# Kernel tuning notes

Hardware: AMD Instinct MI355X
Metric: run time of the kernel (lower is better)

## Reference

```python
import jax, jax.numpy as jnp
import numpy as np

DIM = 384
H = 64
W = 64
NB = 8
BS = DIM // NB
WF = W // 2 + 1
EPS = 1e-5


def _layernorm(x, g, b):
    mu = jnp.mean(x, axis=-1, keepdims=True)
    var = jnp.mean(jnp.square(x - mu), axis=-1, keepdims=True)
    return (x - mu) * jax.lax.rsqrt(var + EPS) * g + b


def setup_inputs() -> dict:
    key = jax.random.key(0)
    ks = jax.random.split(key, 8)
    scale = 0.02
    x = jax.random.normal(ks[0], (8, H, W, DIM), dtype=jnp.float32)
    # complex params stored as real view (..., 2) like torch.view_as_real
    w1 = scale * jax.random.normal(ks[1], (H, WF, NB, BS, BS, 2), dtype=jnp.float32)
    b1 = scale * jax.random.normal(ks[2], (H, WF, NB, BS, 2), dtype=jnp.float32)
    norm1_w = jnp.ones((DIM,), jnp.float32)
    norm1_b = jnp.zeros((DIM,), jnp.float32)
    norm2_w = jnp.ones((DIM,), jnp.float32)
    norm2_b = jnp.zeros((DIM,), jnp.float32)
    lim1 = 1.0 / np.sqrt(DIM)
    lim2 = 1.0 / np.sqrt(4 * DIM)
    mlp_w1 = jax.random.uniform(ks[3], (DIM, 4 * DIM), jnp.float32, -lim1, lim1)
    mlp_b1 = jax.random.uniform(ks[4], (4 * DIM,), jnp.float32, -lim1, lim1)
    mlp_w2 = jax.random.uniform(ks[5], (4 * DIM, DIM), jnp.float32, -lim2, lim2)
    mlp_b2 = jax.random.uniform(ks[6], (DIM,), jnp.float32, -lim2, lim2)
    return {"x": x, "w1": w1, "b1": b1, "norm1_w": norm1_w, "norm1_b": norm1_b,
            "norm2_w": norm2_w, "norm2_b": norm2_b, "mlp_w1": mlp_w1, "mlp_b1": mlp_b1,
            "mlp_w2": mlp_w2, "mlp_b2": mlp_b2}


def reference(x, w1, b1, norm1_w, norm1_b, norm2_w, norm2_b, mlp_w1, mlp_b1, mlp_w2, mlp_b2):
    B, h, w, C = x.shape
    residual = x
    xn = _layernorm(x, norm1_w, norm1_b)
    # spectral token mixing (fp32, ortho norm)
    xf = jnp.fft.rfft2(xn.astype(jnp.float32), axes=(1, 2), norm="ortho")  # (B,H,WF,C) complex
    xf = xf.reshape(B, h, w // 2 + 1, NB, BS)
    w1c = jax.lax.complex(w1[..., 0], w1[..., 1])  # (H,WF,NB,BS,BS)
    b1c = jax.lax.complex(b1[..., 0], b1[..., 1])  # (H,WF,NB,BS)
    o1 = jnp.einsum("bhwni,hwnio->bhwno", xf, w1c) + b1c
    o1 = jax.lax.complex(jax.nn.relu(o1.real), jax.nn.relu(o1.imag))
    o1 = o1.reshape(B, h, w // 2 + 1, C)
    xs = jnp.fft.irfft2(o1, s=(h, w), axes=(1, 2), norm="ortho")  # (B,H,W,C) real
    # channel MLP (dropout in eval mode = identity), exact GELU as torch default
    xm = _layernorm(xs, norm2_w, norm2_b)
    hdn = jax.nn.gelu(xm @ mlp_w1 + mlp_b1, approximate=False)
    mlp_out = hdn @ mlp_w2 + mlp_b2
    return xs + residual + mlp_out
```

## Files before the change

### kernel.cpp

```cpp
#include <hip/hip_runtime.h>
#include <math.h>


#define BB 8
#define CC 384
#define WF 33
#define NBK 8
#define BSZ 48
#define NTOK 32768
#define TW64 0.09817477042468103f

#define T_AWF 0
#define T_AHF 5120
#define T_AHI 21504
#define T_AWI 37888

typedef __attribute__((ext_vector_type(8))) short bf16x8;
typedef __attribute__((ext_vector_type(4))) float f32x4;

__device__ __forceinline__ unsigned short f2b(float f) {
  union { float f; unsigned u; } x; x.f = f;
  unsigned u = x.u;
  return (unsigned short)((u + 0x7fffu + ((u >> 16) & 1u)) >> 16);
}
__device__ __forceinline__ float b2fl(unsigned short u) {
  return __uint_as_float(((unsigned)u) << 16);
}
__device__ __forceinline__ void gload16(const void* g, void* l) {
  __builtin_amdgcn_global_load_lds(
      (const __attribute__((address_space(1))) void*)g,
      (__attribute__((address_space(3))) void*)l, 16, 0, 0);
}

__global__ __launch_bounds__(256) void prep_kernel(unsigned short* __restrict__ A,
    const float* __restrict__ mw1, unsigned short* __restrict__ w1t,
    const float* __restrict__ mw2, unsigned short* __restrict__ w2t) {
  __shared__ float tile[32][33];
  int bid = blockIdx.x;
  if (bid < 64) {
    int idx0 = bid * 256 + threadIdx.x;
    const float S = 0.125f;
    for (int e = idx0; e < 5120; e += 16384) {
      int m = e >> 6, w = e & 63;
      float val = 0.f;
      if (m < 66) {
        int kwv = m >> 1;
        float th = (float)((kwv * w) & 63) * TW64;
        val = (m & 1) ? (((kwv==0)||(kwv==32)) ? 0.f : -sinf(th)*S) : cosf(th)*S;
      }
      A[T_AWF + e] = f2b(val);
    }
    for (int e = idx0; e < 16384; e += 16384) {
      int comp = e >> 13; int r = e & 8191; int mp = r >> 6, hh = r & 63;
      int cpo = mp >> 6, kh = mp & 63;
      float th = (float)((kh * hh) & 63) * TW64;
      float cv = cosf(th), sv = sinf(th);
      float fv = (cpo == 0) ? (comp == 0 ? cv : sv) : (comp == 0 ? -sv : cv);
      A[T_AHF + e] = f2b(fv * S);
      float iv = (cpo == 0) ? (comp == 0 ? cv : -sv) : (comp == 0 ? sv : cv);
      A[T_AHI + e] = f2b(iv * S);
    }
    for (int e = idx0; e < 4096; e += 16384) {
      int w = e >> 6, kp = e & 63;
      float val;
      if (kp <= 32) {
        float th = (float)((kp * w) & 63) * TW64;
        val = cosf(th) * (((kp==0)||(kp==32)) ? 1.f : 2.f) * S;
      } else {
        int k2 = kp - 32;
        float th = (float)((k2 * w) & 63) * TW64;
        val = -2.f * sinf(th) * S;
      }
      A[T_AWI + e] = f2b(val);
    }
    return;
  }
  const float* in; unsigned short* outb; int R, C, tb;
  if (bid < 640) { in = mw1; outb = w1t; R = 384; C = 1536; tb = bid - 64; }
  else           { in = mw2; outb = w2t; R = 1536; C = 384; tb = bid - 640; }
  int ntc = C >> 5;
  int bx = tb % ntc;
  int by = tb / ntc;
  int tx = threadIdx.x & 31, ty = threadIdx.x >> 5;
  for (int rr2 = ty; rr2 < 32; rr2 += 8)
    tile[rr2][tx] = in[(size_t)(by*32+rr2)*C + bx*32 + tx];
  __syncthreads();
  for (int rr2 = ty; rr2 < 32; rr2 += 8)
    outb[(size_t)(bx*32+rr2)*R + by*32 + tx] = f2b(tile[tx][rr2]);
}

__global__ __launch_bounds__(256) void ln1t_kernel(const float* __restrict__ x,
    const float* __restrict__ g, const float* __restrict__ be,
    unsigned short* __restrict__ xn) {
  int outer = blockIdx.x;
  int tid = threadIdx.x, lane = tid & 63, wg = tid >> 6;
  const float* base = x + (size_t)outer * 64 * 384;
  float s[16], s2[16];
#pragma unroll
  for (int q = 0; q < 16; ++q) { s[q] = 0.f; s2[q] = 0.f; }
  for (int ch = 0; ch < 6; ++ch) {
#pragma unroll
    for (int q = 0; q < 16; ++q) {
      float v = base[(size_t)(wg*16 + q)*384 + ch*64 + lane];
      s[q] += v; s2[q] += v*v;
    }
  }
#pragma unroll
  for (int q = 0; q < 16; ++q) {
#pragma unroll
    for (int off = 32; off >= 1; off >>= 1) {
      s[q] += __shfl_xor(s[q], off);
      s2[q] += __shfl_xor(s2[q], off);
    }
  }
  float mu[16], rs[16];
#pragma unroll
  for (int q = 0; q < 16; ++q) {
    mu[q] = s[q] * (1.f/384.f);
    rs[q] = rsqrtf(s2[q] * (1.f/384.f) - mu[q]*mu[q] + 1e-5f);
  }
  unsigned short* o = xn + (size_t)outer * 384 * 64;
  for (int ch = 0; ch < 6; ++ch) {
    int c = ch*64 + lane;
    float ga = g[c], bb2 = be[c];
#pragma unroll
    for (int qq = 0; qq < 4; ++qq) {
      unsigned short hv[4];
#pragma unroll
      for (int r2 = 0; r2 < 4; ++r2) {
        int q = qq*4 + r2;
        hv[r2] = f2b((base[(size_t)(wg*16+q)*384 + c]-mu[q])*rs[q]*ga + bb2);
      }
      uint2 pw;
      pw.x = hv[0] | ((unsigned)hv[1] << 16);
      pw.y = hv[2] | ((unsigned)hv[3] << 16);
      *(uint2*)(o + (size_t)c*64 + wg*16 + qq*4) = pw;
    }
  }
}

template<int STAGE>
__global__ __launch_bounds__(256) void dft_kernel(
    const unsigned short* __restrict__ A0, const unsigned short* __restrict__ D,
    unsigned short* __restrict__ O) {
  constexpr int M = (STAGE==0) ? 80 : (STAGE==3) ? 64 : 128;
  constexpr int MT = M / 16;
  constexpr int NA = (STAGE==1 || STAGE==2) ? 2 : 1;
  constexpr int ABYTES = NA * M * 128;
  constexpr int STG = ABYTES + 16384;
  constexpr int EPB = 64 * 128 * 4;
  constexpr int SB = (STG > EPB) ? STG : EPB;
  __shared__ __align__(16) char smem[SB];
  char* BPL = smem + ABYTES;

  int bid = blockIdx.x;
  int cc = bid % 3; int outer = bid / 3;
  int c0 = cc * 128;
  int tid = threadIdx.x, lane = tid & 63, wid = tid >> 6;
  int rr = lane & 15, rq = lane >> 4;
  int b, h = 0, kw = 0;
  if (STAGE == 0 || STAGE == 3) { b = outer >> 6; h = outer & 63; }
  else { b = outer / 33; kw = outer % 33; }

  f32x4 acc[MT][2];
#pragma unroll
  for (int mt = 0; mt < MT; ++mt)
#pragma unroll
    for (int nt = 0; nt < 2; ++nt) acc[mt][nt] = (f32x4){0.f,0.f,0.f,0.f};

  const unsigned short* Atab =
    (STAGE==0) ? A0+T_AWF : (STAGE==1) ? A0+T_AHF : (STAGE==2) ? A0+T_AHI : A0+T_AWI;
  constexpr int ACH = NA * M * 8;
#pragma unroll
  for (int i = 0; i < (ACH + 255)/256; ++i) {
    int t2 = tid + i*256;
    if ((ACH % 256 == 0) || (t2 < ACH)) {
      int mm = t2 >> 3, ch = t2 & 7;
      gload16(Atab + mm*64 + ((ch ^ (mm & 7)) << 3), smem + i*4096 + wid*1024);
    }
  }

  int ncomp = (STAGE == 1) ? ((kw == 0 || kw == 32) ? 1 : 2) : NA;

  for (int comp = 0; comp < ncomp; ++comp) {
    if (comp) __syncthreads();
    if (STAGE == 0) {
      const unsigned short* src = D + (((size_t)(b*64 + h))*384 + c0) * 64;
#pragma unroll
      for (int i = 0; i < 4; ++i) {
        int idx = tid + i*256;
        int c = idx >> 3, ch = idx & 7;
        gload16(src + c*64 + ((ch ^ (c & 7)) << 3), BPL + i*4096 + wid*1024);
      }
    } else {
      size_t P; int RS;
      if (STAGE == 1) { P = (size_t)b*(64*66*384) + (size_t)(2*kw + comp)*384 + c0; RS = 66*384; }
      else if (STAGE == 2) { P = ((size_t)((b*2 + comp)*33) + kw)*64*384 + c0; RS = 384; }
      else { P = (size_t)b*(64*64*384) + (size_t)h*384 + c0; RS = 64*384; }
      const unsigned short* p0 = D + P;
#pragma unroll
      for (int i = 0; i < 4; ++i) {
        int kq = (tid >> 6) + i*4;
        int c2 = (tid & 63) * 2;
        const unsigned short* p = p0 + (size_t)(4*kq)*RS + c2;
        unsigned u0 = *(const unsigned*)p;
        unsigned u1 = *(const unsigned*)(p + RS);
        unsigned u2 = *(const unsigned*)(p + 2*(size_t)RS);
        unsigned u3 = *(const unsigned*)(p + 3*(size_t)RS);
        uint2 w0, w1v;
        w0.x = (u0 & 0xffffu) | (u1 << 16);
        w0.y = (u2 & 0xffffu) | (u3 << 16);
        w1v.x = (u0 >> 16) | (u1 & 0xffff0000u);
        w1v.y = (u2 >> 16) | (u3 & 0xffff0000u);
        *(uint2*)(BPL + c2*128 + ((kq*8) ^ ((c2 & 7) << 4))) = w0;
        *(uint2*)(BPL + (c2+1)*128 + ((kq*8) ^ (((c2+1) & 7) << 4))) = w1v;
      }
    }
    __syncthreads();
#pragma unroll
    for (int kh2 = 0; kh2 < 2; ++kh2) {
      int chb = kh2*4 + rq;
      bf16x8 bfr[2];
#pragma unroll
      for (int nt = 0; nt < 2; ++nt) {
        int n = wid*32 + nt*16 + rr;
        bfr[nt] = *(const bf16x8*)(BPL + n*128 + ((chb ^ (n & 7)) << 4));
      }
#pragma unroll
      for (int mt = 0; mt < MT; ++mt) {
        int mr = mt*16 + rr;
        bf16x8 af = *(const bf16x8*)(smem + comp*(M*128) + mr*128 + ((chb ^ (mr & 7)) << 4));
#pragma unroll
        for (int nt = 0; nt < 2; ++nt)
          acc[mt][nt] = __builtin_amdgcn_mfma_f32_16x16x32_bf16(af, bfr[nt], acc[mt][nt], 0, 0, 0);
      }
    }
  }
  __syncthreads();

  float* ep = (float*)smem;
  constexpr int NHM = (M + 63) / 64;
#pragma unroll
  for (int hm = 0; hm < NHM; ++hm) {
    if (hm) __syncthreads();
#pragma unroll
    for (int mo = 0; mo < 4; ++mo) {
      int mt = hm*4 + mo;
      if (mt >= MT) break;
#pragma unroll
      for (int nt = 0; nt < 2; ++nt)
#pragma unroll
        for (int j = 0; j < 4; ++j) {
          int m2 = mo*16 + rq*4 + j;
          int cl = wid*32 + nt*16 + rr;
          ep[m2*128 + (cl ^ ((m2 & 7) << 2))] = acc[mt][nt][j];
        }
    }
    __syncthreads();
    for (int it = tid; it < 64*16; it += 256) {
      int m2 = it >> 4, u8 = it & 15;
      int m = hm*64 + m2;
      if (m >= M) break;
      if (STAGE == 0 && m >= 66) break;
      if (STAGE == 2) { int cp = m >> 6; if (cp && (kw == 0 || kw == 32)) continue; }
      int swz = (m2 & 7) << 2;
      float4 v0 = *(const float4*)(ep + m2*128 + ((u8*8) ^ swz));
      float4 v1 = *(const float4*)(ep + m2*128 + ((u8*8 + 4) ^ swz));
      uint4 pw;
      pw.x = f2b(v0.x) | ((unsigned)f2b(v0.y) << 16);
      pw.y = f2b(v0.z) | ((unsigned)f2b(v0.w) << 16);
      pw.z = f2b(v1.x) | ((unsigned)f2b(v1.y) << 16);
      pw.w = f2b(v1.z) | ((unsigned)f2b(v1.w) << 16);
      size_t rowb;
      if (STAGE == 0) rowb = ((size_t)(b*64 + h)*66 + m)*384 + c0;
      else if (STAGE == 1) { int cp = m >> 6, kh = m & 63;
        rowb = (((size_t)((b*2 + cp)*64 + kh)*33) + kw)*384 + c0; }
      else if (STAGE == 2) { int cp = m >> 6, h2 = m & 63; int kp = cp ? 32 + kw : kw;
        rowb = ((size_t)(b*64 + kp)*64 + h2)*384 + c0; }
      else rowb = ((size_t)(b*64 + h)*64 + m)*384 + c0;
      *(uint4*)(O + rowb + u8*8) = pw;
    }
  }
}

__global__ __launch_bounds__(384) void blockmm2_kernel(
    const unsigned short* __restrict__ S2, const float* __restrict__ w1,
    const float* __restrict__ b1, unsigned short* __restrict__ o1) {
  int bid = blockIdx.x;
  int np = bid % 4;
  int kw = (bid / 4) % WF;
  int h = bid / (4*WF);
  int tid = threadIdx.x;
  __shared__ float4 wl4[2][48*24];
  __shared__ float2 xl[2][BB][48];
  __shared__ float2 bl[2][48];
#pragma unroll
  for (int e = tid; e < 2304; e += 384) {
    int sub = e / 1152, r = e % 1152;
    const float4* wb4 = (const float4*)(w1 + ((size_t)((h*WF + kw)*NBK) + 2*np + sub)*(BSZ*BSZ*2));
    wl4[sub][r] = wb4[r];
  }
  if (tid < 96) {
    int sub = tid / 48, o = tid % 48;
    bl[sub][o] = ((const float2*)b1)[((size_t)((h*WF + kw)*NBK) + 2*np + sub)*BSZ + o];
  }
#pragma unroll
  for (int e = tid; e < 768; e += 384) {
    int sub = e / 384, r = e % 384, bb = r / 48, i = r % 48;
    int n = 2*np + sub;
    size_t ir = (((size_t)((bb*2 + 0)*64 + h)*33) + kw)*384 + n*48 + i;
    size_t ii = (((size_t)((bb*2 + 1)*64 + h)*33) + kw)*384 + n*48 + i;
    xl[sub][bb][i] = make_float2(b2fl(S2[ir]), b2fl(S2[ii]));
  }
  __syncthreads();
  int sub = tid / 192, r = tid % 192, bb = r / 24, o2 = r % 24;
  float4 bv = *(const float4*)(&bl[sub][2*o2]);
  float2 a0 = make_float2(bv.x, bv.y);
  float2 a1 = make_float2(bv.z, bv.w);
#pragma unroll
  for (int i = 0; i < 48; ++i) {
    float2 xv = xl[sub][bb][i];
    float4 wv = wl4[sub][i*24 + o2];
    a0.x += xv.x*wv.x - xv.y*wv.y;
    a0.y += xv.x*wv.y + xv.y*wv.x;
    a1.x += xv.x*wv.z - xv.y*wv.w;
    a1.y += xv.x*wv.w + xv.y*wv.z;
  }
  int n = 2*np + sub;
  size_t idr = (((size_t)((bb*2 + 0)*33) + kw)*64 + h)*384 + n*48 + 2*o2;
  size_t idi = (((size_t)((bb*2 + 1)*33) + kw)*64 + h)*384 + n*48 + 2*o2;
  *(unsigned*)(o1 + idr) = f2b(fmaxf(a0.x, 0.f)) | ((unsigned)f2b(fmaxf(a1.x, 0.f)) << 16);
  *(unsigned*)(o1 + idi) = f2b(fmaxf(a0.y, 0.f)) | ((unsigned)f2b(fmaxf(a1.y, 0.f)) << 16);
}

__global__ __launch_bounds__(256) void ln2_kernel(const unsigned short* __restrict__ in,
    const float* __restrict__ g, const float* __restrict__ bsh,
    unsigned short* __restrict__ outp) {
  int token = blockIdx.x * 4 + (threadIdx.x >> 6);
  int lane = threadIdx.x & 63;
  const unsigned short* row = in + (size_t)token * CC;
  float v[6]; float s = 0.f;
#pragma unroll
  for (int j = 0; j < 6; ++j) { v[j] = b2fl(row[lane + 64*j]); s += v[j]; }
#pragma unroll
  for (int off = 32; off >= 1; off >>= 1) s += __shfl_xor(s, off);
  float mu = s * (1.0f/CC);
  float q = 0.f;
#pragma unroll
  for (int j = 0; j < 6; ++j) { float d = v[j] - mu; q += d*d; }
#pragma unroll
  for (int off = 32; off >= 1; off >>= 1) q += __shfl_xor(q, off);
  float rs = rsqrtf(q * (1.0f/CC) + 1e-5f);
#pragma unroll
  for (int j = 0; j < 6; ++j) {
    int c = lane + 64*j;
    outp[(size_t)token*CC + c] = f2b((v[j]-mu)*rs*g[c] + bsh[c]);
  }
}

template<int MODE>
__global__ __launch_bounds__(256) void mfma_gemm_kernel(
    const unsigned short* __restrict__ A, int lda,
    const unsigned short* __restrict__ BT, int ldbt,
    const float* __restrict__ bias,
    void* __restrict__ Cp, int ldc, int K, int ntn,
    const unsigned short* __restrict__ xsb, const float* __restrict__ xres,
    const float* __restrict__ b2v) {
  __shared__ __align__(16) unsigned short gsm[128*64*2];
  unsigned short* As = gsm;
  unsigned short* Bs = gsm + 128*64;
  int nb = (int)gridDim.x;
  int bidx = (int)blockIdx.x;
  int bswz = (bidx & 7) * (nb >> 3) + (bidx >> 3);
  int bn = bswz % ntn;
  int bm = bswz / ntn;
  int t = threadIdx.x;
  int lane = t & 63;
  int wid = t >> 6;
  int wm = wid >> 1, wn = wid & 1;
  int rr = lane & 15, rq = lane >> 4;

  f32x4 acc[4][4];
#pragma unroll
  for (int m = 0; m < 4; ++m)
#pragma unroll
    for (int n = 0; n < 4; ++n) acc[m][n] = (f32x4){0.f,0.f,0.f,0.f};

  const unsigned short* Abase = A + (size_t)bm*128*lda;
  const unsigned short* Bbase = BT + (size_t)bn*128*ldbt;

  for (int k0 = 0; k0 < K; k0 += 64) {
#pragma unroll
    for (int i = 0; i < 4; ++i) {
      int idx = t + i*256;
      int row = idx >> 3, ch = idx & 7;
      gload16(Abase + (size_t)row*lda + k0 + ((ch ^ (row & 7)) << 3),
              (char*)As + i*4096 + wid*1024);
    }
#pragma unroll
    for (int i = 0; i < 4; ++i) {
      int idx = t + i*256;
      int row = idx >> 3, ch = idx & 7;
      gload16(Bbase + (size_t)row*ldbt + k0 + ((ch ^ (row & 7)) << 3),
              (char*)Bs + i*4096 + wid*1024);
    }
    __syncthreads();
#pragma unroll
    for (int ks = 0; ks < 2; ++ks) {
      int chb = ks*4 + rq;
      bf16x8 af[4], bfr[4];
#pragma unroll
      for (int m = 0; m < 4; ++m) {
        int row = wm*64 + m*16 + rr;
        af[m] = *(const bf16x8*)((const char*)As + row*128 + ((chb ^ (row & 7)) << 4));
      }
#pragma unroll
      for (int n = 0; n < 4; ++n) {
        int row = wn*64 + n*16 + rr;
        bfr[n] = *(const bf16x8*)((const char*)Bs + row*128 + ((chb ^ (row & 7)) << 4));
      }
#pragma unroll
      for (int m = 0; m < 4; ++m)
#pragma unroll
        for (int n = 0; n < 4; ++n)
          acc[m][n] = __builtin_amdgcn_mfma_f32_16x16x32_bf16(af[m], bfr[n], acc[m][n], 0, 0, 0);
    }
    __syncthreads();
  }

  if (MODE == 0) {
    unsigned short* ep = gsm;
#pragma unroll
    for (int m = 0; m < 4; ++m)
#pragma unroll
      for (int n = 0; n < 4; ++n)
#pragma unroll
        for (int j = 0; j < 4; ++j) {
          int row = wm*64 + m*16 + rq*4 + j;
          int col = wn*64 + n*16 + rr;
          float v = acc[m][n][j];
          v += bias[bn*128 + col];
          v = 0.5f*v*(1.f + erff(v*0.70710678118654752f));
          ep[row*128 + (col ^ ((row & 7) << 3))] = f2b(v);
        }
    __syncthreads();
    for (int it = t; it < 128*16; it += 256) {
      int m = it >> 4, u8 = it & 15;
      uint4 pw = *(const uint4*)(ep + m*128 + ((u8*8) ^ ((m & 7) << 3)));
      *(uint4*)((unsigned short*)Cp + (size_t)(bm*128 + m)*ldc + bn*128 + u8*8) = pw;
    }
  } else {
    float* ep = (float*)gsm;
#pragma unroll
    for (int half = 0; half < 2; ++half) {
      __syncthreads();
#pragma unroll
      for (int mo = 0; mo < 2; ++mo) {
        int m = half*2 + mo;
#pragma unroll
        for (int n = 0; n < 4; ++n)
#pragma unroll
          for (int j = 0; j < 4; ++j) {
            int lr = wm*32 + mo*16 + rq*4 + j;
            int col = wn*64 + n*16 + rr;
            ep[lr*128 + (col ^ ((lr & 7) << 2))] = acc[m][n][j];
          }
      }
      __syncthreads();
      for (int it = t; it < 64*32; it += 256) {
        int lr = it >> 5, u = it & 31;
        int swz = (lr & 7) << 2;
        float4 v = *(const float4*)(ep + lr*128 + ((u*4) ^ swz));
        int grow = bm*128 + (lr >> 5)*64 + (half*2 + ((lr >> 4) & 1))*16 + (lr & 15);
        int gcol = bn*128 + u*4;
        size_t idx = (size_t)grow*ldc + gcol;
        float4 xr = *(const float4*)(xres + idx);
        uint2 xsv = *(const uint2*)(xsb + idx);
        float4 bv = *(const float4*)(b2v + gcol);
        float4 ov;
        ov.x = v.x + xr.x + b2fl((unsigned short)(xsv.x & 0xffffu)) + bv.x;
        ov.y = v.y + xr.y + b2fl((unsigned short)(xsv.x >> 16)) + bv.y;
        ov.z = v.z + xr.z + b2fl((unsigned short)(xsv.y & 0xffffu)) + bv.z;
        ov.w = v.w + xr.w + b2fl((unsigned short)(xsv.y >> 16)) + bv.w;
        *(float4*)((float*)Cp + idx) = ov;
      }
    }
  }
}

extern "C" void kernel_launch(void* const* d_in, const int* in_sizes, int n_in,
                              void* d_out, int out_size, void* d_ws, size_t ws_size,
                              hipStream_t stream) {
  const float* x   = (const float*)d_in[0];
  const float* w1  = (const float*)d_in[1];
  const float* b1  = (const float*)d_in[2];
  const float* n1w = (const float*)d_in[3];
  const float* n1b = (const float*)d_in[4];
  const float* n2w = (const float*)d_in[5];
  const float* n2b = (const float*)d_in[6];
  const float* mw1 = (const float*)d_in[7];
  const float* mb1 = (const float*)d_in[8];
  const float* mw2 = (const float*)d_in[9];
  const float* mb2 = (const float*)d_in[10];
  float* out = (float*)d_out;

  char* ws = (char*)d_ws;
  const size_t MB = 1ull << 20;
  unsigned short* xn  = (unsigned short*)(ws + 0*MB);
  unsigned short* S1  = (unsigned short*)(ws + 26*MB);
  unsigned short* S2  = (unsigned short*)(ws + 53*MB);
  unsigned short* o1  = (unsigned short*)(ws + 80*MB);
  unsigned short* S3  = (unsigned short*)(ws + 107*MB);
  unsigned short* xsb = (unsigned short*)(ws + 133*MB);
  unsigned short* xmb = (unsigned short*)(ws + 159*MB);
  unsigned short* hid = (unsigned short*)(ws + 185*MB);
  unsigned short* w1t = (unsigned short*)(ws + 286*MB);
  unsigned short* w2t = (unsigned short*)(ws + 288*MB);
  unsigned short* atab = (unsigned short*)(ws + 290*MB);

  prep_kernel<<<1216, 256, 0, stream>>>(atab, mw1, w1t, mw2, w2t);

  ln1t_kernel<<<512, 256, 0, stream>>>(x, n1w, n1b, xn);
  dft_kernel<0><<<512*3, 256, 0, stream>>>(atab, xn, S1);
  dft_kernel<1><<<264*3, 256, 0, stream>>>(atab, S1, S2);
  blockmm2_kernel<<<64*WF*4, 384, 0, stream>>>(S2, w1, b1, o1);
  dft_kernel<2><<<264*3, 256, 0, stream>>>(atab, o1, S3);
  dft_kernel<3><<<512*3, 256, 0, stream>>>(atab, S3, xsb);
  ln2_kernel<<<NTOK/4, 256, 0, stream>>>(xsb, n2w, n2b, xmb);
  mfma_gemm_kernel<0><<<256*12, 256, 0, stream>>>(xmb, 384, w1t, 384, mb1,
                                                  hid, 1536, 384, 12,
                                                  nullptr, nullptr, nullptr);
  mfma_gemm_kernel<1><<<256*3, 256, 0, stream>>>(hid, 1536, w2t, 1536, nullptr,
                                                 out, 384, 1536, 3,
                                                 xsb, x, mb2);
}
```

Baseline: 386.3 us.

## Fold LayerNorm2 into MLP GEMM epilogue and double-buffer GEMM K loop

Replaces the ln2 kernel, which wrote a normalized bf16 tensor, with a stats-only kernel that stores per-token mean and rstd. The first GEMM now reads the raw xsb directly. The gamma scaling is folded into the transposed W1 weights, and gamma·W1 column sums plus the beta/bias term are precomputed in prep, so normalization is applied algebraically in the GEMM epilogue. The GEMM main loop also changes from single-buffered 64-wide K tiles to double-buffered 32-wide tiles, overlapping loads with MFMA. This removes one full activation write/read pass, at the cost of using E[x²]-μ² for variance and a serial 384-step column-sum loop in prep.

```diff
diff --git a/kernel.cpp b/kernel.cpp
--- a/kernel.cpp
+++ b/kernel.cpp
@@ -34,7 +34,9 @@
 
 __global__ __launch_bounds__(256) void prep_kernel(unsigned short* __restrict__ A,
     const float* __restrict__ mw1, unsigned short* __restrict__ w1t,
-    const float* __restrict__ mw2, unsigned short* __restrict__ w2t) {
+    const float* __restrict__ mw2, unsigned short* __restrict__ w2t,
+    const float* __restrict__ n2w, const float* __restrict__ n2b,
+    const float* __restrict__ mb1, float2* __restrict__ gsbb) {
   __shared__ float tile[32][33];
   int bid = blockIdx.x;
   if (bid < 64) {
@@ -75,9 +77,22 @@
     }
     return;
   }
-  const float* in; unsigned short* outb; int R, C, tb;
-  if (bid < 640) { in = mw1; outb = w1t; R = 384; C = 1536; tb = bid - 64; }
-  else           { in = mw2; outb = w2t; R = 1536; C = 384; tb = bid - 640; }
+  if (bid >= 1216) {
+    int n0 = (bid - 1216) * 256 + threadIdx.x;
+    if (n0 < 1536) {
+      float gsv = 0.f, bbv = 0.f;
+      for (int k = 0; k < 384; ++k) {
+        float a = mw1[(size_t)k*1536 + n0];
+        gsv += n2w[k]*a;
+        bbv += n2b[k]*a;
+      }
+      gsbb[n0] = make_float2(gsv, bbv + mb1[n0]);
+    }
+    return;
+  }
+  const float* in; unsigned short* outb; int R, C, tb; bool fold;
+  if (bid < 640) { in = mw1; outb = w1t; R = 384; C = 1536; tb = bid - 64; fold = true; }
+  else           { in = mw2; outb = w2t; R = 1536; C = 384; tb = bid - 640; fold = false; }
   int ntc = C >> 5;
   int bx = tb % ntc;
   int by = tb / ntc;
@@ -85,8 +100,9 @@
   for (int rr2 = ty; rr2 < 32; rr2 += 8)
     tile[rr2][tx] = in[(size_t)(by*32+rr2)*C + bx*32 + tx];
   __syncthreads();
+  float gv = fold ? n2w[by*32 + tx] : 1.f;
   for (int rr2 = ty; rr2 < 32; rr2 += 8)
-    outb[(size_t)(bx*32+rr2)*R + by*32 + tx] = f2b(tile[tx][rr2]);
+    outb[(size_t)(bx*32+rr2)*R + by*32 + tx] = f2b(tile[tx][rr2] * gv);
 }
 
 __global__ __launch_bounds__(256) void ln1t_kernel(const float* __restrict__ x,
@@ -333,28 +349,26 @@
   *(unsigned*)(o1 + idi) = f2b(fmaxf(a0.y, 0.f)) | ((unsigned)f2b(fmaxf(a1.y, 0.f)) << 16);
 }
 
-__global__ __launch_bounds__(256) void ln2_kernel(const unsigned short* __restrict__ in,
-    const float* __restrict__ g, const float* __restrict__ bsh,
-    unsigned short* __restrict__ outp) {
+__global__ __launch_bounds__(256) void stats_kernel(const unsigned short* __restrict__ in,
+    float2* __restrict__ stats) {
   int token = blockIdx.x * 4 + (threadIdx.x >> 6);
   int lane = threadIdx.x & 63;
   const unsigned short* row = in + (size_t)token * CC;
-  float v[6]; float s = 0.f;
-#pragma unroll
-  for (int j = 0; j < 6; ++j) { v[j] = b2fl(row[lane + 64*j]); s += v[j]; }
-#pragma unroll
-  for (int off = 32; off >= 1; off >>= 1) s += __shfl_xor(s, off);
-  float mu = s * (1.0f/CC);
-  float q = 0.f;
-#pragma unroll
-  for (int j = 0; j < 6; ++j) { float d = v[j] - mu; q += d*d; }
-#pragma unroll
-  for (int off = 32; off >= 1; off >>= 1) q += __shfl_xor(q, off);
-  float rs = rsqrtf(q * (1.0f/CC) + 1e-5f);
+  float s = 0.f, s2 = 0.f;
 #pragma unroll
   for (int j = 0; j < 6; ++j) {
-    int c = lane + 64*j;
-    outp[(size_t)token*CC + c] = f2b((v[j]-mu)*rs*g[c] + bsh[c]);
+    float v = b2fl(row[lane + 64*j]);
+    s += v; s2 += v*v;
+  }
+#pragma unroll
+  for (int off = 32; off >= 1; off >>= 1) {
+    s += __shfl_xor(s, off);
+    s2 += __shfl_xor(s2, off);
+  }
+  if (lane == 0) {
+    float mu = s * (1.0f/CC);
+    float rs = rsqrtf(s2 * (1.0f/CC) - mu*mu + 1e-5f);
+    stats[token] = make_float2(mu, rs);
   }
 }
 
@@ -362,13 +376,11 @@
 __global__ __launch_bounds__(256) void mfma_gemm_kernel(
     const unsigned short* __restrict__ A, int lda,
     const unsigned short* __restrict__ BT, int ldbt,
-    const float* __restrict__ bias,
     void* __restrict__ Cp, int ldc, int K, int ntn,
+    const float2* __restrict__ stats, const float2* __restrict__ gsbb,
     const unsigned short* __restrict__ xsb, const float* __restrict__ xres,
     const float* __restrict__ b2v) {
-  __shared__ __align__(16) unsigned short gsm[128*64*2];
-  unsigned short* As = gsm;
-  unsigned short* Bs = gsm + 128*64;
+  __shared__ __align__(16) char gsm[32768];
   int nb = (int)gridDim.x;
   int bidx = (int)blockIdx.x;
   int bswz = (bidx & 7) * (nb >> 3) + (bidx >> 3);
@@ -388,61 +400,79 @@
 
   const unsigned short* Abase = A + (size_t)bm*128*lda;
   const unsigned short* Bbase = BT + (size_t)bn*128*ldbt;
-
-  for (int k0 = 0; k0 < K; k0 += 64) {
-#pragma unroll
-    for (int i = 0; i < 4; ++i) {
-      int idx = t + i*256;
-      int row = idx >> 3, ch = idx & 7;
-      gload16(Abase + (size_t)row*lda + k0 + ((ch ^ (row & 7)) << 3),
-              (char*)As + i*4096 + wid*1024);
-    }
-#pragma unroll
-    for (int i = 0; i < 4; ++i) {
-      int idx = t + i*256;
-      int row = idx >> 3, ch = idx & 7;
-      gload16(Bbase + (size_t)row*ldbt + k0 + ((ch ^ (row & 7)) << 3),
-              (char*)Bs + i*4096 + wid*1024);
-    }
+  int nt = K >> 5;
+
+#define STG(bsel, t0)                                                        \
+  {                                                                          \
+    _Pragma("unroll")                                                        \
+    for (int i = 0; i < 2; ++i) {                                            \
+      int u = t + i*256;                                                     \
+      int row = u >> 2, ch = u & 3;                                          \
+      gload16(Abase + (size_t)row*lda + (t0)*32 + ((ch ^ (row & 3)) << 3),   \
+              gsm + (bsel)*16384 + i*4096 + wid*1024);                       \
+      gload16(Bbase + (size_t)row*ldbt + (t0)*32 + ((ch ^ (row & 3)) << 3),  \
+              gsm + (bsel)*16384 + 8192 + i*4096 + wid*1024);                \
+    }                                                                        \
+  }
+
+#define CMP(bsel)                                                            \
+  {                                                                          \
+    const char* Ab2 = gsm + (bsel)*16384;                                    \
+    const char* Bb2 = Ab2 + 8192;                                            \
+    bf16x8 af[4], bfv[4];                                                    \
+    _Pragma("unroll")                                                        \
+    for (int m = 0; m < 4; ++m) {                                            \
+      int row = wm*64 + m*16 + rr;                                           \
+      af[m] = *(const bf16x8*)(Ab2 + row*64 + ((rq ^ (row & 3)) << 4));      \
+    }                                                                        \
+    _Pragma("unroll")                                                        \
+    for (int n = 0; n < 4; ++n) {                                            \
+      int row = wn*64 + n*16 + rr;                                           \
+      bfv[n] = *(const bf16x8*)(Bb2 + row*64 + ((rq ^ (row & 3)) << 4));     \
+    }                                                                        \
+    _Pragma("unroll")                                                        \
+    for (int m = 0; m < 4; ++m)                                              \
+      _Pragma("unroll")                                                      \
+      for (int n = 0; n < 4; ++n)                                            \
+        acc[m][n] = __builtin_amdgcn_mfma_f32_16x16x32_bf16(af[m], bfv[n], acc[m][n], 0, 0, 0); \
+  }
+
+  STG(0, 0);
+  __syncthreads();
+  int cur = 0;
+  for (int tt = 0; tt < nt - 1; ++tt) {
+    STG(cur ^ 1, tt + 1);
+    CMP(cur);
     __syncthreads();
-#pragma unroll
-    for (int ks = 0; ks < 2; ++ks) {
-      int chb = ks*4 + rq;
-      bf16x8 af[4], bfr[4];
-#pragma unroll
-      for (int m = 0; m < 4; ++m) {
-        int row = wm*64 + m*16 + rr;
-        af[m] = *(const bf16x8*)((const char*)As + row*128 + ((chb ^ (row & 7)) << 4));
-      }
+    cur ^= 1;
+  }
+  CMP(cur);
+  __syncthreads();
+
+#undef STG
+#undef CMP
+
+  if (MODE == 0) {
+    unsigned short* ep = (unsigned short*)gsm;
+#pragma unroll
+    for (int m = 0; m < 4; ++m) {
+      float2 st[4];
+#pragma unroll
+      for (int j = 0; j < 4; ++j)
+        st[j] = stats[bm*128 + wm*64 + m*16 + rq*4 + j];
 #pragma unroll
       for (int n = 0; n < 4; ++n) {
-        int row = wn*64 + n*16 + rr;
-        bfr[n] = *(const bf16x8*)((const char*)Bs + row*128 + ((chb ^ (row & 7)) << 4));
-      }
-#pragma unroll
-      for (int m = 0; m < 4; ++m)
-#pragma unroll
-        for (int n = 0; n < 4; ++n)
-          acc[m][n] = __builtin_amdgcn_mfma_f32_16x16x32_bf16(af[m], bfr[n], acc[m][n], 0, 0, 0);
-    }
-    __syncthreads();
-  }
-
-  if (MODE == 0) {
-    unsigned short* ep = gsm;
-#pragma unroll
-    for (int m = 0; m < 4; ++m)
-#pragma unroll
-      for (int n = 0; n < 4; ++n)
+        int lcol = wn*64 + n*16 + rr;
+        float2 gb = gsbb[bn*128 + lcol];
 #pragma unroll
         for (int j = 0; j < 4; ++j) {
+          float v = st[j].y * acc[m][n][j] - st[j].y * st[j].x * gb.x + gb.y;
+          v = 0.5f*v*(1.f + erff(v*0.70710678118654752f));
           int row = wm*64 + m*16 + rq*4 + j;
-          int col = wn*64 + n*16 + rr;
-          float v = acc[m][n][j];
-          v += bias[bn*128 + col];
-          v = 0.5f*v*(1.f + erff(v*0.70710678118654752f));
-          ep[row*128 + (col ^ ((row & 7) << 3))] = f2b(v);
+          ep[row*128 + (lcol ^ ((row & 7) << 3))] = f2b(v);
         }
+      }
+    }
     __syncthreads();
     for (int it = t; it < 128*16; it += 256) {
       int m = it >> 4, u8 = it & 15;
@@ -512,13 +542,14 @@
   unsigned short* o1  = (unsigned short*)(ws + 80*MB);
   unsigned short* S3  = (unsigned short*)(ws + 107*MB);
   unsigned short* xsb = (unsigned short*)(ws + 133*MB);
-  unsigned short* xmb = (unsigned short*)(ws + 159*MB);
+  float2*         stats = (float2*)(ws + 159*MB);
   unsigned short* hid = (unsigned short*)(ws + 185*MB);
   unsigned short* w1t = (unsigned short*)(ws + 286*MB);
   unsigned short* w2t = (unsigned short*)(ws + 288*MB);
   unsigned short* atab = (unsigned short*)(ws + 290*MB);
-
-  prep_kernel<<<1216, 256, 0, stream>>>(atab, mw1, w1t, mw2, w2t);
+  float2*         gsbb = (float2*)(ws + 292*MB);
+
+  prep_kernel<<<1222, 256, 0, stream>>>(atab, mw1, w1t, mw2, w2t, n2w, n2b, mb1, gsbb);
 
   ln1t_kernel<<<512, 256, 0, stream>>>(x, n1w, n1b, xn);
   dft_kernel<0><<<512*3, 256, 0, stream>>>(atab, xn, S1);
@@ -526,11 +557,11 @@
   blockmm2_kernel<<<64*WF*4, 384, 0, stream>>>(S2, w1, b1, o1);
   dft_kernel<2><<<264*3, 256, 0, stream>>>(atab, o1, S3);
   dft_kernel<3><<<512*3, 256, 0, stream>>>(atab, S3, xsb);
-  ln2_kernel<<<NTOK/4, 256, 0, stream>>>(xsb, n2w, n2b, xmb);
-  mfma_gemm_kernel<0><<<256*12, 256, 0, stream>>>(xmb, 384, w1t, 384, mb1,
+  stats_kernel<<<NTOK/4, 256, 0, stream>>>(xsb, stats);
+  mfma_gemm_kernel<0><<<256*12, 256, 0, stream>>>(xsb, 384, w1t, 384,
                                                   hid, 1536, 384, 12,
-                                                  nullptr, nullptr, nullptr);
-  mfma_gemm_kernel<1><<<256*3, 256, 0, stream>>>(hid, 1536, w2t, 1536, nullptr,
+                                                  stats, gsbb, nullptr, nullptr, nullptr);
+  mfma_gemm_kernel<1><<<256*3, 256, 0, stream>>>(hid, 1536, w2t, 1536,
                                                  out, 384, 1536, 3,
-                                                 xsb, x, mb2);
-}
+                                                 nullptr, nullptr, xsb, x, mb2);
+}
```

Result: no change. 385.6 us (-0.2%).
